# Kernel tuning notes

Hardware: AMD Instinct MI355X
Metric: run time of the kernel (lower is better)

## Reference

```python
import jax, jax.numpy as jnp
import numpy as np

D_MODEL = 96
D_INNER = 2 * D_MODEL          # expand=2
D_STATE = 16
D_CONV = 4
DT_RANK = 6                    # ceil(96/16)


def setup_inputs() -> dict:
    key = jax.random.key(0)
    ks = jax.random.split(key, 12)
    B, C, H, W = 4, D_MODEL, 64, 64
    # dt_proj bias init (inverse-softplus of dt sampled log-uniform in [1e-3, 1e-1])
    dtv = jnp.exp(jax.random.uniform(ks[7], (D_INNER,), jnp.float32)
                  * (np.log(0.1) - np.log(0.001)) + np.log(0.001))
    dtv = jnp.clip(dtv, 1e-4, None)
    dt_proj_b = dtv + jnp.log(-jnp.expm1(-dtv))
    dt_std = DT_RANK ** -0.5
    return {
        "x": jax.random.normal(ks[0], (B, C, H, W), jnp.float32),
        "proj_w": jax.random.normal(ks[1], (2 * C, C, 1, 1), jnp.float32) * 0.05,
        "dconv_w": jax.random.normal(ks[2], (C, 2 * C, 3, 3), jnp.float32) * 0.02,
        "in_proj_w": jax.random.normal(ks[3], (2 * D_INNER, C), jnp.float32) * 0.05,
        "conv1d_w": jax.random.normal(ks[4], (D_INNER, D_CONV), jnp.float32) * 0.2,
        "conv1d_b": jnp.zeros((D_INNER,), jnp.float32),
        "x_proj_w": jax.random.normal(ks[5], (DT_RANK + 2 * D_STATE, D_INNER), jnp.float32) * 0.05,
        "dt_proj_w": jax.random.uniform(ks[6], (D_INNER, DT_RANK), jnp.float32, -dt_std, dt_std),
        "dt_proj_b": dt_proj_b,
        "A_log": jnp.log(jnp.tile(jnp.arange(1, D_STATE + 1, dtype=jnp.float32), (D_INNER, 1))),
        "D": jnp.ones((D_INNER,), jnp.float32),
        "out_proj_w": jax.random.normal(ks[8], (C, D_INNER), jnp.float32) * 0.05,
    }


def _cssm_forward(x, proj_w, dconv_w, in_proj_w, conv1d_w, conv1d_b,
                  x_proj_w, dt_proj_w, dt_proj_b, A_log, D, out_proj_w):
    Bsz, Cdim, H, W = x.shape
    L = H * W
    # proj (1x1 conv, no bias) then dconv (3x3 conv, pad 1, no bias)
    xp = jax.lax.conv_general_dilated(x, proj_w, (1, 1), 'VALID',
                                      dimension_numbers=('NCHW', 'OIHW', 'NCHW'))
    xp = jax.lax.conv_general_dilated(xp, dconv_w, (1, 1), ((1, 1), (1, 1)),
                                      dimension_numbers=('NCHW', 'OIHW', 'NCHW'))
    seq = xp.reshape(Bsz, Cdim, L).transpose(0, 2, 1)            # (B, L, C)
    # in_proj (no bias) -> (B, 2*d_inner, L)
    xz = jnp.einsum('blc,ec->bel', seq, in_proj_w)
    xin, z = jnp.split(xz, 2, axis=1)                             # (B, d_inner, L) each
    # causal depthwise conv1d (pad d_conv-1 on left) + SiLU
    xpad = jnp.pad(xin, ((0, 0), (0, 0), (D_CONV - 1, 0)))
    xc = jax.lax.conv_general_dilated(xpad, conv1d_w[:, None, :], (1,), 'VALID',
                                      dimension_numbers=('NCH', 'OIH', 'NCH'),
                                      feature_group_count=D_INNER)
    xc = jax.nn.silu(xc + conv1d_b[None, :, None])                # (B, d_inner, L)
    # x_proj -> dt (rank), B (state), C (state)
    x_dbl = jnp.einsum('bdl,ed->ble', xc, x_proj_w)               # (B, L, rank+2n)
    dt, Bc, Cc = jnp.split(x_dbl, [DT_RANK, DT_RANK + D_STATE], axis=-1)
    delta = jax.nn.softplus(jnp.einsum('blr,dr->bld', dt, dt_proj_w) + dt_proj_b)  # (B,L,d)
    A = -jnp.exp(A_log)                                           # (d, n)
    u = xc.transpose(0, 2, 1)                                     # (B, L, d)
    # selective scan: h_t = exp(delta_t A) * h_{t-1} + delta_t B_t u_t  (diag, per channel/state)
    dA = jnp.exp(delta[..., None] * A)                            # (B,L,d,n)
    dBu = delta[..., None] * Bc[:, :, None, :] * u[..., None]     # (B,L,d,n)

    def combine(c1, c2):
        a1, b1 = c1
        a2, b2 = c2
        return a2 * a1, a2 * b1 + b2

    _, h = jax.lax.associative_scan(combine, (dA, dBu), axis=1)   # (B,L,d,n)
    y = jnp.einsum('bldn,bln->bld', h, Cc) + D * u                # (B,L,d)
    y = y * jax.nn.silu(z.transpose(0, 2, 1))                     # gate
    out = jnp.einsum('bld,cd->blc', y, out_proj_w)                # (B,L,C)
    return out.transpose(0, 2, 1).reshape(Bsz, Cdim, H, W)


def reference(x, proj_w, dconv_w, in_proj_w, conv1d_w, conv1d_b,
              x_proj_w, dt_proj_w, dt_proj_b, A_log, D, out_proj_w):
    return _cssm_forward(x, proj_w, dconv_w, in_proj_w, conv1d_w, conv1d_b,
                         x_proj_w, dt_proj_w, dt_proj_b, A_log, D, out_proj_w)
```

## Files before the change

kernel.cpp:

```cpp
#include <hip/hip_runtime.h>
#include <math.h>

#define LL    4096
#define CDIM  96
#define DIN   192
#define NST   16
#define XE    38

typedef __attribute__((ext_vector_type(8))) short v8s;
typedef __attribute__((ext_vector_type(4))) float v4f;
typedef unsigned short ushort_t;
typedef unsigned int uint_t;

#if __has_builtin(__builtin_amdgcn_exp2f)
__device__ __forceinline__ float fexp2(float x) { return __builtin_amdgcn_exp2f(x); }
#else
__device__ __forceinline__ float fexp2(float x) { return exp2f(x); }
#endif
#if __has_builtin(__builtin_amdgcn_logf)
__device__ __forceinline__ float flog2(float x) { return __builtin_amdgcn_logf(x); }
#else
__device__ __forceinline__ float flog2(float x) { return __log2f(x); }
#endif

__device__ __forceinline__ float siluf(float x) {
    return x * __builtin_amdgcn_rcpf(1.f + fexp2(-1.44269504f * x));
}
__device__ __forceinline__ ushort_t f2bf(float f) {
    uint_t u = __builtin_bit_cast(uint_t, f);
    return (ushort_t)((u + 0x7fffu + ((u >> 16) & 1u)) >> 16);
}

__global__ __launch_bounds__(256) void k_prep(const float* __restrict__ proj_w,
                                              const float* __restrict__ dconv_w,
                                              const float* __restrict__ in_proj_w,
                                              const float* __restrict__ out_proj_w,
                                              const float* __restrict__ x_proj_w,
                                              ushort_t* __restrict__ Wbf,
                                              ushort_t* __restrict__ Wibf,
                                              ushort_t* __restrict__ Wobf,
                                              ushort_t* __restrict__ Wxbf) {
    int i = blockIdx.x * 256 + threadIdx.x;
    if (i < 82944) {
        int k = i % 9;
        int c = (i / 9) % 96;
        int o = i / 864;
        float s = 0.f;
        for (int j = 0; j < 192; ++j)
            s += dconv_w[(o * 192 + j) * 9 + k] * proj_w[j * 96 + c];
        Wbf[(k * 96 + o) * 96 + c] = f2bf(s);
        return;
    }
    i -= 82944;
    if (i < 36864) { Wibf[i] = f2bf(in_proj_w[i]); return; }
    i -= 36864;
    if (i < 18432) { Wobf[i] = f2bf(out_proj_w[i]); return; }
    i -= 18432;
    if (i < 9216) {
        int e = i / 192;
        Wxbf[i] = (e < XE) ? f2bf(x_proj_w[i]) : (ushort_t)0;
    }
}

__global__ __launch_bounds__(256) void k_xpad(const float* __restrict__ x,
                                              ushort_t* __restrict__ xT) {
    int yy = blockIdx.x;
    int b  = blockIdx.y;
    int yv = yy - 1;
    for (int i = threadIdx.x; i < 68 * 12; i += 256) {
        int xx = i % 68, cig = i / 68;
        int xv = xx - 1;
        ushort_t u[8];
        if (yv >= 0 && yv < 64 && xv >= 0 && xv < 64) {
            const float* sp = x + ((size_t)(b * 96 + cig * 8)) * LL + yv * 64 + xv;
#pragma unroll
            for (int j = 0; j < 8; ++j) u[j] = f2bf(sp[j * LL]);
        } else {
#pragma unroll
            for (int j = 0; j < 8; ++j) u[j] = 0;
        }
        uint4 pk;
        pk.x = u[0] | ((uint_t)u[1] << 16); pk.y = u[2] | ((uint_t)u[3] << 16);
        pk.z = u[4] | ((uint_t)u[5] << 16); pk.w = u[6] | ((uint_t)u[7] << 16);
        *(uint4*)(xT + (((size_t)b * 66 + yy) * 68 + xx) * 96 + cig * 8) = pk;
    }
}

__global__ __launch_bounds__(384, 2) void k_convin(const ushort_t* __restrict__ xT,
                                                   const ushort_t* __restrict__ Wbf,
                                                   const ushort_t* __restrict__ Wibf,
                                                   float* __restrict__ xz) {
    __shared__ ushort_t s_seq[32 * 104];
    int tid = threadIdx.x;
    int w = tid >> 6, l = tid & 63;
    int n = l & 15, g = l >> 4;
    int blk = blockIdx.x;
    int b = blk >> 7, rem = blk & 127;
    int y = rem >> 1, half = rem & 1;
    int lx = (w & 1) * 16;
    int x0 = half * 32 + lx;
    int co0 = (w >> 1) * 32;
    v4f acc0 = {0.f, 0.f, 0.f, 0.f};
    v4f acc1 = {0.f, 0.f, 0.f, 0.f};
    const ushort_t* xb = xT + (((size_t)b * 66 + y) * 68 + x0 + n) * 96 + g * 8;
    const ushort_t* aw = Wbf + ((size_t)co0 + n) * 96 + g * 8;
#pragma unroll
    for (int tap = 0; tap < 9; ++tap) {
        int dy = tap / 3, dx = tap % 3;
        const ushort_t* bp = xb + (dy * 68 + dx) * 96;
        const ushort_t* ap = aw + (size_t)tap * 9216;
#pragma unroll
        for (int kk = 0; kk < 3; ++kk) {
            v8s bf = *(const v8s*)(bp + kk * 32);
            v8s a0 = *(const v8s*)(ap + kk * 32);
            v8s a1 = *(const v8s*)(ap + 1536 + kk * 32);
            acc0 = __builtin_amdgcn_mfma_f32_16x16x32_bf16(a0, bf, acc0, 0, 0, 0);
            acc1 = __builtin_amdgcn_mfma_f32_16x16x32_bf16(a1, bf, acc1, 0, 0, 0);
        }
    }
    {
        int ll = lx + n;
        ushort_t* sp = s_seq + ll * 104 + co0 + g * 4;
        ushort4 p0, p1;
        p0.x = f2bf(acc0[0]); p0.y = f2bf(acc0[1]); p0.z = f2bf(acc0[2]); p0.w = f2bf(acc0[3]);
        p1.x = f2bf(acc1[0]); p1.y = f2bf(acc1[1]); p1.z = f2bf(acc1[2]); p1.w = f2bf(acc1[3]);
        *(ushort4*)sp = p0;
        *(ushort4*)(sp + 16) = p1;
    }
    __syncthreads();
    int coh = w * 64;
    v4f acc[4][2];
#pragma unroll
    for (int mt = 0; mt < 4; ++mt)
#pragma unroll
        for (int lt = 0; lt < 2; ++lt) acc[mt][lt] = (v4f){0.f, 0.f, 0.f, 0.f};
    const ushort_t* ap2 = Wibf + ((size_t)coh + n) * 96 + g * 8;
#pragma unroll
    for (int lt = 0; lt < 2; ++lt) {
        const ushort_t* bp2 = s_seq + (lt * 16 + n) * 104 + g * 8;
#pragma unroll
        for (int kk = 0; kk < 3; ++kk) {
            v8s bf = *(const v8s*)(bp2 + kk * 32);
#pragma unroll
            for (int mt = 0; mt < 4; ++mt) {
                v8s af = *(const v8s*)(ap2 + mt * 16 * 96 + kk * 32);
                acc[mt][lt] = __builtin_amdgcn_mfma_f32_16x16x32_bf16(af, bf, acc[mt][lt], 0, 0, 0);
            }
        }
    }
    int l0g = y * 64 + half * 32;
    float* ob = xz + (size_t)b * 384 * LL + l0g + n;
#pragma unroll
    for (int mt = 0; mt < 4; ++mt) {
        int e = coh + mt * 16 + g * 4;
#pragma unroll
        for (int lt = 0; lt < 2; ++lt)
#pragma unroll
            for (int r = 0; r < 4; ++r)
                ob[(size_t)(e + r) * LL + lt * 16] = acc[mt][lt][r];
    }
}

__global__ __launch_bounds__(256) void k_conv1d(const float* __restrict__ xz,
                                                const float* __restrict__ w,
                                                const float* __restrict__ bias,
                                                float* __restrict__ xc,
                                                ushort_t* __restrict__ xcT) {
    int tid = threadIdx.x;
    int d_l = tid >> 2, tg = tid & 3;
    int b = blockIdx.z, dg = blockIdx.y, tt = blockIdx.x;
    int d = dg * 64 + d_l;
    int t0 = tt * 16 + tg * 4;
    const float* xin = xz + (size_t)(b * 384 + d) * LL;
    float4 cur = *(const float4*)(xin + t0);
    float pm3 = 0.f, pm2 = 0.f, pm1 = 0.f;
    if (t0 > 0) {
        float4 prev = *(const float4*)(xin + t0 - 4);
        pm3 = prev.y; pm2 = prev.z; pm1 = prev.w;
    }
    float in[7] = {pm3, pm2, pm1, cur.x, cur.y, cur.z, cur.w};
    float w0 = w[d * 4 + 0], w1 = w[d * 4 + 1], w2 = w[d * 4 + 2], w3 = w[d * 4 + 3];
    float bb = bias[d];
    float o[4];
#pragma unroll
    for (int i = 0; i < 4; ++i) {
        float s = bb + w0 * in[i] + w1 * in[i + 1] + w2 * in[i + 2] + w3 * in[i + 3];
        o[i] = siluf(s);
    }
    float4 ov; ov.x = o[0]; ov.y = o[1]; ov.z = o[2]; ov.w = o[3];
    *(float4*)(xc + (size_t)(b * DIN + d) * LL + t0) = ov;
    ushort_t* xt = xcT + ((size_t)b * 4096 + t0) * DIN + d;
#pragma unroll
    for (int i = 0; i < 4; ++i)
        xt[(size_t)i * DIN] = f2bf(o[i]);
}

__global__ __launch_bounds__(256, 4) void k_xprojm(const ushort_t* __restrict__ xcT,
                                                   const ushort_t* __restrict__ Wxbf,
                                                   float* __restrict__ dtT,
                                                   float* __restrict__ BtP,
                                                   float* __restrict__ CtP) {
    int tid = threadIdx.x;
    int w = tid >> 6, l = tid & 63;
    int n = l & 15, g = l >> 4;
    int b = blockIdx.y;
    int l0 = blockIdx.x * 64 + w * 16;
    const ushort_t* bp = xcT + ((size_t)b * 4096 + l0 + n) * 192 + g * 8;
    const ushort_t* ap = Wxbf + (size_t)n * 192 + g * 8;
    v4f acc[3];
#pragma unroll
    for (int m = 0; m < 3; ++m) acc[m] = (v4f){0.f, 0.f, 0.f, 0.f};
#pragma unroll
    for (int kk = 0; kk < 6; ++kk) {
        v8s bf = *(const v8s*)(bp + kk * 32);
#pragma unroll
        for (int m = 0; m < 3; ++m) {
            v8s af = *(const v8s*)(ap + m * 16 * 192 + kk * 32);
            acc[m] = __builtin_amdgcn_mfma_f32_16x16x32_bf16(af, bf, acc[m], 0, 0, 0);
        }
    }
    float* dtb = dtT + (size_t)b * 6 * LL + l0 + n;
    float* Bb = BtP + ((size_t)b * LL + l0 + n) * 16;
    float* Cb = CtP + ((size_t)b * LL + l0 + n) * 16;
#pragma unroll
    for (int m = 0; m < 3; ++m)
#pragma unroll
        for (int r = 0; r < 4; ++r) {
            int e = m * 16 + g * 4 + r;
            float v = acc[m][r];
            if (e < 6)       dtb[(size_t)e * LL] = v;
            else if (e < 22) Bb[e - 6] = v;
            else if (e < 38) Cb[e - 22] = v;
        }
}

__global__ __launch_bounds__(256) void k_dtproj(const float* __restrict__ dtT,
                                                const float* __restrict__ dtw,
                                                const float* __restrict__ dtb,
                                                float* __restrict__ delta) {
    int tx = threadIdx.x, ty = threadIdx.y;
    int b = blockIdx.y;
    int l = blockIdx.x * 64 + tx;
    int d0 = blockIdx.z * 48 + ty * 12;
    const float* dbase = dtT + (size_t)b * 6 * LL + l;
    float r0 = dbase[0], r1 = dbase[LL], r2 = dbase[2 * LL];
    float r3 = dbase[3 * LL], r4 = dbase[4 * LL], r5 = dbase[5 * LL];
#pragma unroll
    for (int j = 0; j < 12; ++j) {
        int dd = d0 + j;
        const float* wr2 = dtw + dd * 6;
        float s = dtb[dd] + wr2[0] * r0 + wr2[1] * r1 + wr2[2] * r2
                          + wr2[3] * r3 + wr2[4] * r4 + wr2[5] * r5;
        float e = fexp2(s * 1.44269504f);
        float sp = 0.69314718f * flog2(1.f + e);
        delta[((size_t)b * DIN + dd) * LL + l] = sp;
    }
}

__global__ __launch_bounds__(512, 6) void k_scan(const float* __restrict__ delta,
                                                 const float* __restrict__ xc,
                                                 const float* __restrict__ BtP,
                                                 const float* __restrict__ CtP,
                                                 const float* __restrict__ A_log,
                                                 const float* __restrict__ Dp,
                                                 float* __restrict__ xz) {
    __shared__ float s_d[32 * 132];
    __shared__ float s_u[32 * 132];
    __shared__ float s_a[32][17];
    __shared__ float s_h[32][17];
    int tid = threadIdx.x;
    int n = tid & 15, cg = tid >> 4;
    int bd = blockIdx.x;
    int d = bd % DIN, b = bd / DIN;
    const float* drow = delta + (size_t)(b * DIN + d) * LL;
    const float* urow = xc    + (size_t)(b * DIN + d) * LL;
    const float* zrow = xz    + (size_t)(b * 384 + DIN + d) * LL;
    ushort_t* ygb     = (ushort_t*)(xz + (size_t)b * 384 * LL);
    float A2 = -__expf(A_log[d * NST + n]) * 1.44269504f;
    float Dd = Dp[d];

    {
        int t8 = tid * 8;
        int li = ((t8 >> 7) * 132) + (t8 & 127);
        *(float4*)&s_d[li]     = *(const float4*)(drow + t8);
        *(float4*)&s_d[li + 4] = *(const float4*)(drow + t8 + 4);
        *(float4*)&s_u[li]     = *(const float4*)(urow + t8);
        *(float4*)&s_u[li + 4] = *(const float4*)(urow + t8 + 4);
    }
    __syncthreads();

    int t0 = cg * 128;
    int lb = cg * 132;
    const float* pB = BtP + ((size_t)b * LL + t0) * 16 + n;
    const float* pC = CtP + ((size_t)b * LL + t0) * 16 + n;

    float h = 0.f, sdu = 0.f;
    float4 du_c = *(float4*)&s_d[lb];
    float4 u_c  = *(float4*)&s_u[lb];
    float B0 = pB[0], B1 = pB[16], B2 = pB[32], B3 = pB[48];
    for (int s = 0; s < 31; ++s) {
        int ln = lb + s * 4 + 4;
        const float* pBn = pB + s * 64 + 64;
        float4 du_n = *(float4*)&s_d[ln];
        float4 u_n  = *(float4*)&s_u[ln];
        float Bn0 = pBn[0], Bn1 = pBn[16], Bn2 = pBn[32], Bn3 = pBn[48];
        float a0 = fexp2(du_c.x * A2), a1 = fexp2(du_c.y * A2);
        float a2 = fexp2(du_c.z * A2), a3 = fexp2(du_c.w * A2);
        h = fmaf(a0, h, (du_c.x * u_c.x) * B0);
        h = fmaf(a1, h, (du_c.y * u_c.y) * B1);
        h = fmaf(a2, h, (du_c.z * u_c.z) * B2);
        h = fmaf(a3, h, (du_c.w * u_c.w) * B3);
        sdu += (du_c.x + du_c.y) + (du_c.z + du_c.w);
        du_c = du_n; u_c = u_n; B0 = Bn0; B1 = Bn1; B2 = Bn2; B3 = Bn3;
    }
    {
        float a0 = fexp2(du_c.x * A2), a1 = fexp2(du_c.y * A2);
        float a2 = fexp2(du_c.z * A2), a3 = fexp2(du_c.w * A2);
        h = fmaf(a0, h, (du_c.x * u_c.x) * B0);
        h = fmaf(a1, h, (du_c.y * u_c.y) * B1);
        h = fmaf(a2, h, (du_c.z * u_c.z) * B2);
        h = fmaf(a3, h, (du_c.w * u_c.w) * B3);
        sdu += (du_c.x + du_c.y) + (du_c.z + du_c.w);
    }
    s_a[cg][n] = fexp2(sdu * A2);
    s_h[cg][n] = h;
    __syncthreads();

    {
        int l = tid & 63, w = tid >> 6;
        int c = l & 31, nn = (w << 1) | (l >> 5);
        float a  = s_a[c][nn];
        float hh = s_h[c][nn];
#pragma unroll
        for (int st = 1; st < 32; st <<= 1) {
            float ap = __shfl_up(a, st, 32);
            float hp = __shfl_up(hh, st, 32);
            bool ok = (c >= st);
            hh = ok ? fmaf(a, hp, hh) : hh;
            a  = ok ? a * ap : a;
        }
        float h0 = __shfl_up(hh, 1, 32);
        if (c == 0) h0 = 0.f;
        s_a[c][nn] = h0;
    }
    __syncthreads();

    h = s_a[cg][n];
    const int j = n & 3;
    const bool e1 = (j == 1), e2 = (j == 2), e3 = (j == 3);
    du_c = *(float4*)&s_d[lb];
    u_c  = *(float4*)&s_u[lb];
    B0 = pB[0]; B1 = pB[16]; B2 = pB[32]; B3 = pB[48];
    float C0 = pC[0], C1 = pC[16], C2 = pC[32], C3 = pC[48];
    float4 z_c = *(const float4*)(zrow + t0);
    for (int s = 0; s < 32; ++s) {
        float4 du_n, u_n, z_n;
        float Bn0, Bn1, Bn2, Bn3, Cn0, Cn1, Cn2, Cn3;
        if (s < 31) {
            int ln = lb + s * 4 + 4;
            const float* pBn = pB + s * 64 + 64;
            const float* pCn = pC + s * 64 + 64;
            du_n = *(float4*)&s_d[ln];
            u_n  = *(float4*)&s_u[ln];
            Bn0 = pBn[0]; Bn1 = pBn[16]; Bn2 = pBn[32]; Bn3 = pBn[48];
            Cn0 = pCn[0]; Cn1 = pCn[16]; Cn2 = pCn[32]; Cn3 = pCn[48];
            z_n = *(const float4*)(zrow + t0 + s * 4 + 4);
        }
        float a0 = fexp2(du_c.x * A2), a1 = fexp2(du_c.y * A2);
        float a2 = fexp2(du_c.z * A2), a3 = fexp2(du_c.w * A2);
        h = fmaf(a0, h, (du_c.x * u_c.x) * B0); float p0 = h * C0;
        h = fmaf(a1, h, (du_c.y * u_c.y) * B1); float p1 = h * C1;
        h = fmaf(a2, h, (du_c.z * u_c.z) * B2); float p2 = h * C2;
        h = fmaf(a3, h, (du_c.w * u_c.w) * B3); float p3 = h * C3;
        p0 += __shfl_xor(p0, 1); p0 += __shfl_xor(p0, 2);
        p1 += __shfl_xor(p1, 1); p1 += __shfl_xor(p1, 2);
        p2 += __shfl_xor(p2, 1); p2 += __shfl_xor(p2, 2);
        p3 += __shfl_xor(p3, 1); p3 += __shfl_xor(p3, 2);
        float pj = e3 ? p3 : (e2 ? p2 : (e1 ? p1 : p0));
        pj += __shfl_xor(pj, 4); pj += __shfl_xor(pj, 8);
        float uj = e3 ? u_c.w : (e2 ? u_c.z : (e1 ? u_c.y : u_c.x));
        float zj = e3 ? z_c.w : (e2 ? z_c.z : (e1 ? z_c.y : z_c.x));
        float yj = fmaf(Dd, uj, pj) * siluf(zj);
        if (n < 4)
            ygb[(size_t)(t0 + s * 4 + n) * DIN + d] = f2bf(yj);
        du_c = du_n; u_c = u_n; z_c = z_n;
        B0 = Bn0; B1 = Bn1; B2 = Bn2; B3 = Bn3;
        C0 = Cn0; C1 = Cn1; C2 = Cn2; C3 = Cn3;
    }
}

__global__ __launch_bounds__(512, 2) void k_outproj(const float* __restrict__ xzBase,
                                                    const ushort_t* __restrict__ Wobf,
                                                    float* __restrict__ out) {
    int tid = threadIdx.x;
    int w = tid >> 6, l = tid & 63;
    int n = l & 15, g = l >> 4;
    int b = blockIdx.y;
    int l0 = blockIdx.x * 64 + (w >> 1) * 16;
    int c0 = (w & 1) * 48;
    const ushort_t* ygb = (const ushort_t*)(xzBase + (size_t)b * 384 * LL);
    const ushort_t* bp = ygb + ((size_t)l0 + n) * 192 + g * 8;
    const ushort_t* ap = Wobf + ((size_t)c0 + n) * 192 + g * 8;
    v4f acc[3];
#pragma unroll
    for (int m = 0; m < 3; ++m) acc[m] = (v4f){0.f, 0.f, 0.f, 0.f};
#pragma unroll
    for (int kk = 0; kk < 6; ++kk) {
        v8s bf = *(const v8s*)(bp + kk * 32);
#pragma unroll
        for (int m = 0; m < 3; ++m) {
            v8s af = *(const v8s*)(ap + m * 16 * 192 + kk * 32);
            acc[m] = __builtin_amdgcn_mfma_f32_16x16x32_bf16(af, bf, acc[m], 0, 0, 0);
        }
    }
    float* ob = out + (size_t)b * 96 * LL + l0 + n;
#pragma unroll
    for (int m = 0; m < 3; ++m)
#pragma unroll
        for (int r = 0; r < 4; ++r)
            ob[(size_t)(c0 + m * 16 + g * 4 + r) * LL] = acc[m][r];
}

extern "C" void kernel_launch(void* const* d_in, const int* in_sizes, int n_in,
                              void* d_out, int out_size, void* d_ws, size_t ws_size,
                              hipStream_t stream) {
    const float* x         = (const float*)d_in[0];
    const float* proj_w    = (const float*)d_in[1];
    const float* dconv_w   = (const float*)d_in[2];
    const float* in_proj_w = (const float*)d_in[3];
    const float* conv1d_w  = (const float*)d_in[4];
    const float* conv1d_b  = (const float*)d_in[5];
    const float* x_proj_w  = (const float*)d_in[6];
    const float* dt_proj_w = (const float*)d_in[7];
    const float* dt_proj_b = (const float*)d_in[8];
    const float* A_log     = (const float*)d_in[9];
    const float* Dp        = (const float*)d_in[10];
    const float* out_proj_w= (const float*)d_in[11];
    float* out = (float*)d_out;
    float* ws  = (float*)d_ws;

    ushort_t* Wbf  = (ushort_t*)ws;
    ushort_t* Wibf = (ushort_t*)(ws + 41472);
    ushort_t* Wobf = (ushort_t*)(ws + 59904);
    ushort_t* Wxbf = (ushort_t*)(ws + 69120);
    ushort_t* xT   = (ushort_t*)(ws + 73728);
    float* xz   = ws + 1721856;
    float* xc   = xz + 6291456;
    float* dtT  = xc + 3145728;
    float* BtP  = dtT + 98304;
    float* CtP  = BtP + 262144;
    float* delta= CtP + 262144;
    ushort_t* xcT = (ushort_t*)delta;

    k_prep<<<dim3(576), dim3(256), 0, stream>>>(proj_w, dconv_w, in_proj_w, out_proj_w,
                                                x_proj_w, Wbf, Wibf, Wobf, Wxbf);
    k_xpad<<<dim3(66, 4), dim3(256), 0, stream>>>(x, xT);
    k_convin<<<dim3(512), dim3(384), 0, stream>>>(xT, Wbf, Wibf, xz);
    k_conv1d<<<dim3(256, 3, 4), dim3(256), 0, stream>>>(xz, conv1d_w, conv1d_b, xc, xcT);
    k_xprojm<<<dim3(64, 4), dim3(256), 0, stream>>>(xcT, Wxbf, dtT, BtP, CtP);
    k_dtproj<<<dim3(64, 4, 4), dim3(64, 4), 0, stream>>>(dtT, dt_proj_w, dt_proj_b, delta);
    k_scan<<<dim3(768), dim3(512), 0, stream>>>(delta, xc, BtP, CtP, A_log, Dp, xz);
    k_outproj<<<dim3(64, 4), dim3(512), 0, stream>>>(xz, Wobf, out);
}
```

Before: 129.7 us.

## Fuse dt_proj into scan, merge xpad into prep, transpose gated output layout

Drops the separate dt_proj kernel: each scan block now recomputes softplus(dt_proj) for its channel from the low-rank dtT rows, so the full delta tensor is never written to or read from global memory. The x padding/transposition work is folded into the prep kernel as extra blocks, removing one launch. The scan now writes gated outputs channel-major with contiguous stores instead of strided scattered stores, and out_proj transposes them through shared memory before the MFMA. The costs are redundant dt projection math in every scan block and an extra LDS transpose in out_proj.

```diff
diff --git a/kernel.cpp b/kernel.cpp
--- a/kernel.cpp
+++ b/kernel.cpp
@@ -36,36 +36,39 @@
                                               const float* __restrict__ in_proj_w,
                                               const float* __restrict__ out_proj_w,
                                               const float* __restrict__ x_proj_w,
+                                              const float* __restrict__ x,
                                               ushort_t* __restrict__ Wbf,
                                               ushort_t* __restrict__ Wibf,
                                               ushort_t* __restrict__ Wobf,
-                                              ushort_t* __restrict__ Wxbf) {
-    int i = blockIdx.x * 256 + threadIdx.x;
-    if (i < 82944) {
-        int k = i % 9;
-        int c = (i / 9) % 96;
-        int o = i / 864;
-        float s = 0.f;
-        for (int j = 0; j < 192; ++j)
-            s += dconv_w[(o * 192 + j) * 9 + k] * proj_w[j * 96 + c];
-        Wbf[(k * 96 + o) * 96 + c] = f2bf(s);
+                                              ushort_t* __restrict__ Wxbf,
+                                              ushort_t* __restrict__ xT) {
+    int bid = blockIdx.x;
+    if (bid < 576) {
+        int i = bid * 256 + threadIdx.x;
+        if (i < 82944) {
+            int k = i % 9;
+            int c = (i / 9) % 96;
+            int o = i / 864;
+            float s = 0.f;
+            for (int j = 0; j < 192; ++j)
+                s += dconv_w[(o * 192 + j) * 9 + k] * proj_w[j * 96 + c];
+            Wbf[(k * 96 + o) * 96 + c] = f2bf(s);
+            return;
+        }
+        i -= 82944;
+        if (i < 36864) { Wibf[i] = f2bf(in_proj_w[i]); return; }
+        i -= 36864;
+        if (i < 18432) { Wobf[i] = f2bf(out_proj_w[i]); return; }
+        i -= 18432;
+        if (i < 9216) {
+            int e = i / 192;
+            Wxbf[i] = (e < XE) ? f2bf(x_proj_w[i]) : (ushort_t)0;
+        }
         return;
     }
-    i -= 82944;
-    if (i < 36864) { Wibf[i] = f2bf(in_proj_w[i]); return; }
-    i -= 36864;
-    if (i < 18432) { Wobf[i] = f2bf(out_proj_w[i]); return; }
-    i -= 18432;
-    if (i < 9216) {
-        int e = i / 192;
-        Wxbf[i] = (e < XE) ? f2bf(x_proj_w[i]) : (ushort_t)0;
-    }
-}
-
-__global__ __launch_bounds__(256) void k_xpad(const float* __restrict__ x,
-                                              ushort_t* __restrict__ xT) {
-    int yy = blockIdx.x;
-    int b  = blockIdx.y;
+    int bid2 = bid - 576;
+    int yy = bid2 % 66;
+    int b  = bid2 / 66;
     int yv = yy - 1;
     for (int i = threadIdx.x; i < 68 * 12; i += 256) {
         int xx = i % 68, cig = i / 68;
@@ -234,30 +237,9 @@
         }
 }
 
-__global__ __launch_bounds__(256) void k_dtproj(const float* __restrict__ dtT,
-                                                const float* __restrict__ dtw,
-                                                const float* __restrict__ dtb,
-                                                float* __restrict__ delta) {
-    int tx = threadIdx.x, ty = threadIdx.y;
-    int b = blockIdx.y;
-    int l = blockIdx.x * 64 + tx;
-    int d0 = blockIdx.z * 48 + ty * 12;
-    const float* dbase = dtT + (size_t)b * 6 * LL + l;
-    float r0 = dbase[0], r1 = dbase[LL], r2 = dbase[2 * LL];
-    float r3 = dbase[3 * LL], r4 = dbase[4 * LL], r5 = dbase[5 * LL];
-#pragma unroll
-    for (int j = 0; j < 12; ++j) {
-        int dd = d0 + j;
-        const float* wr2 = dtw + dd * 6;
-        float s = dtb[dd] + wr2[0] * r0 + wr2[1] * r1 + wr2[2] * r2
-                          + wr2[3] * r3 + wr2[4] * r4 + wr2[5] * r5;
-        float e = fexp2(s * 1.44269504f);
-        float sp = 0.69314718f * flog2(1.f + e);
-        delta[((size_t)b * DIN + dd) * LL + l] = sp;
-    }
-}
-
-__global__ __launch_bounds__(512, 6) void k_scan(const float* __restrict__ delta,
+__global__ __launch_bounds__(512, 6) void k_scan(const float* __restrict__ dtT,
+                                                 const float* __restrict__ dtw,
+                                                 const float* __restrict__ dtpb,
                                                  const float* __restrict__ xc,
                                                  const float* __restrict__ BtP,
                                                  const float* __restrict__ CtP,
@@ -272,18 +254,37 @@
     int n = tid & 15, cg = tid >> 4;
     int bd = blockIdx.x;
     int d = bd % DIN, b = bd / DIN;
-    const float* drow = delta + (size_t)(b * DIN + d) * LL;
-    const float* urow = xc    + (size_t)(b * DIN + d) * LL;
-    const float* zrow = xz    + (size_t)(b * 384 + DIN + d) * LL;
-    ushort_t* ygb     = (ushort_t*)(xz + (size_t)b * 384 * LL);
+    const float* urow = xc + (size_t)(b * DIN + d) * LL;
+    const float* zrow = xz + (size_t)(b * 384 + DIN + d) * LL;
+    ushort_t* ygr     = (ushort_t*)(xz + (size_t)b * 384 * LL) + (size_t)d * LL;
     float A2 = -__expf(A_log[d * NST + n]) * 1.44269504f;
     float Dd = Dp[d];
 
     {
         int t8 = tid * 8;
         int li = ((t8 >> 7) * 132) + (t8 & 127);
-        *(float4*)&s_d[li]     = *(const float4*)(drow + t8);
-        *(float4*)&s_d[li + 4] = *(const float4*)(drow + t8 + 4);
+        const float* dt0 = dtT + (size_t)b * 6 * LL + t8;
+        v4f ra[6], rb[6];
+#pragma unroll
+        for (int r = 0; r < 6; ++r) {
+            ra[r] = *(const v4f*)(dt0 + r * LL);
+            rb[r] = *(const v4f*)(dt0 + r * LL + 4);
+        }
+        const float* wr = dtw + d * 6;
+        float w0 = wr[0], w1 = wr[1], w2 = wr[2], w3 = wr[3], w4 = wr[4], w5 = wr[5];
+        float bb = dtpb[d];
+        v4f spa, spb;
+#pragma unroll
+        for (int j = 0; j < 4; ++j) {
+            float s1 = bb + w0 * ra[0][j] + w1 * ra[1][j] + w2 * ra[2][j]
+                          + w3 * ra[3][j] + w4 * ra[4][j] + w5 * ra[5][j];
+            spa[j] = 0.69314718f * flog2(1.f + fexp2(s1 * 1.44269504f));
+            float s2 = bb + w0 * rb[0][j] + w1 * rb[1][j] + w2 * rb[2][j]
+                          + w3 * rb[3][j] + w4 * rb[4][j] + w5 * rb[5][j];
+            spb[j] = 0.69314718f * flog2(1.f + fexp2(s2 * 1.44269504f));
+        }
+        *(v4f*)&s_d[li]     = spa;
+        *(v4f*)&s_d[li + 4] = spb;
         *(float4*)&s_u[li]     = *(const float4*)(urow + t8);
         *(float4*)&s_u[li + 4] = *(const float4*)(urow + t8 + 4);
     }
@@ -382,7 +383,7 @@
         float zj = e3 ? z_c.w : (e2 ? z_c.z : (e1 ? z_c.y : z_c.x));
         float yj = fmaf(Dd, uj, pj) * siluf(zj);
         if (n < 4)
-            ygb[(size_t)(t0 + s * 4 + n) * DIN + d] = f2bf(yj);
+            ygr[t0 + s * 4 + n] = f2bf(yj);
         du_c = du_n; u_c = u_n; z_c = z_n;
         B0 = Bn0; B1 = Bn1; B2 = Bn2; B3 = Bn3;
         C0 = Cn0; C1 = Cn1; C2 = Cn2; C3 = Cn3;
@@ -392,14 +393,33 @@
 __global__ __launch_bounds__(512, 2) void k_outproj(const float* __restrict__ xzBase,
                                                     const ushort_t* __restrict__ Wobf,
                                                     float* __restrict__ out) {
+    __shared__ ushort_t s_yg[64][216];
     int tid = threadIdx.x;
+    int b = blockIdx.y;
+    int l0 = blockIdx.x * 64;
+    const ushort_t* ygb = (const ushort_t*)(xzBase + (size_t)b * 384 * LL);
+    {
+        int q = tid & 63, o = tid >> 6;
+        if (q < 48) {
+            uint4 v[4];
+#pragma unroll
+            for (int jj = 0; jj < 4; ++jj)
+                v[jj] = *(const uint4*)(ygb + (size_t)(q * 4 + jj) * LL + l0 + o * 8);
+            const ushort_t* vs = (const ushort_t*)v;
+#pragma unroll
+            for (int j2 = 0; j2 < 8; ++j2) {
+                ushort4 pk;
+                pk.x = vs[j2]; pk.y = vs[8 + j2]; pk.z = vs[16 + j2]; pk.w = vs[24 + j2];
+                *(ushort4*)&s_yg[o * 8 + j2][q * 4] = pk;
+            }
+        }
+    }
+    __syncthreads();
     int w = tid >> 6, l = tid & 63;
     int n = l & 15, g = l >> 4;
-    int b = blockIdx.y;
-    int l0 = blockIdx.x * 64 + (w >> 1) * 16;
+    int lt = (w >> 1) * 16;
     int c0 = (w & 1) * 48;
-    const ushort_t* ygb = (const ushort_t*)(xzBase + (size_t)b * 384 * LL);
-    const ushort_t* bp = ygb + ((size_t)l0 + n) * 192 + g * 8;
+    const ushort_t* bp = &s_yg[lt + n][g * 8];
     const ushort_t* ap = Wobf + ((size_t)c0 + n) * 192 + g * 8;
     v4f acc[3];
 #pragma unroll
@@ -413,7 +433,7 @@
             acc[m] = __builtin_amdgcn_mfma_f32_16x16x32_bf16(af, bf, acc[m], 0, 0, 0);
         }
     }
-    float* ob = out + (size_t)b * 96 * LL + l0 + n;
+    float* ob = out + (size_t)b * 96 * LL + l0 + lt + n;
 #pragma unroll
     for (int m = 0; m < 3; ++m)
 #pragma unroll
@@ -449,16 +469,14 @@
     float* dtT  = xc + 3145728;
     float* BtP  = dtT + 98304;
     float* CtP  = BtP + 262144;
-    float* delta= CtP + 262144;
-    ushort_t* xcT = (ushort_t*)delta;
-
-    k_prep<<<dim3(576), dim3(256), 0, stream>>>(proj_w, dconv_w, in_proj_w, out_proj_w,
-                                                x_proj_w, Wbf, Wibf, Wobf, Wxbf);
-    k_xpad<<<dim3(66, 4), dim3(256), 0, stream>>>(x, xT);
+    ushort_t* xcT = (ushort_t*)(CtP + 262144);
+
+    k_prep<<<dim3(840), dim3(256), 0, stream>>>(proj_w, dconv_w, in_proj_w, out_proj_w,
+                                                x_proj_w, x, Wbf, Wibf, Wobf, Wxbf, xT);
     k_convin<<<dim3(512), dim3(384), 0, stream>>>(xT, Wbf, Wibf, xz);
     k_conv1d<<<dim3(256, 3, 4), dim3(256), 0, stream>>>(xz, conv1d_w, conv1d_b, xc, xcT);
     k_xprojm<<<dim3(64, 4), dim3(256), 0, stream>>>(xcT, Wxbf, dtT, BtP, CtP);
-    k_dtproj<<<dim3(64, 4, 4), dim3(64, 4), 0, stream>>>(dtT, dt_proj_w, dt_proj_b, delta);
-    k_scan<<<dim3(768), dim3(512), 0, stream>>>(delta, xc, BtP, CtP, A_log, Dp, xz);
+    k_scan<<<dim3(768), dim3(512), 0, stream>>>(dtT, dt_proj_w, dt_proj_b, xc, BtP, CtP,
+                                                A_log, Dp, xz);
     k_outproj<<<dim3(64, 4), dim3(512), 0, stream>>>(xz, Wobf, out);
 }
```

Result: faster. 115.5 us (-10.9%).
